# Performance work log

Measured on AMD Instinct MI355X. Metric: run time of the kernel, lower is better.

## Reference

```python
import jax, jax.numpy as jnp
import numpy as np
import math

EPS = 1e-6
NOISE = 1e-5

def _icnn(x, w0r, b0, w1r, b1, zw, g0r, g1r, ob):
    # x: [..., D]; returns [..., P, D]
    w0 = jax.nn.softplus(w0r) ** 2            # [P, 2D, D]
    w1 = jax.nn.softplus(w1r) ** 2            # [P, D, 2D]
    g0 = jax.nn.sigmoid(g0r)[:, None]          # [P, 1]
    g1 = jax.nn.sigmoid(g1r)[:, None]
    z0 = jax.nn.softplus((jnp.einsum('...d,pkd->...pk', x, w0) + b0) * g0)  # [..., P, 2D]
    xw1 = jnp.einsum('...pk,pdk->...pd', z0, w1) + b1                        # [..., P, D]
    zmap = jnp.einsum('...pk,pkd->...pd', z0, zw)
    z1 = jax.nn.softplus(xw1 * g1 + zmap)
    return z1 + ob

def _convex_gate(x, gw, gb):
    u = jax.nn.softplus(jnp.einsum('...d,od->...o', x, gw) + gb)
    return 1.0 - jnp.exp(-u)  # [..., 1]

def _scalar_hull(x, w0r, b0, w1r, b1, zw, g0r, g1r, ob, gw, gb, key):
    g = _convex_gate(x, gw, gb)
    xg = (x + jax.random.normal(key, x.shape, x.dtype) * NOISE) * g
    r = jnp.sqrt(jnp.mean(xg * xg, axis=-1, keepdims=True) + EPS)
    tau = jnp.exp(0.30343 * r + 0.22159)
    scores = _icnn(xg, w0r, b0, w1r, b1, zw, g0r, g1r, ob).mean(-1)  # [..., P]
    lse = jax.nn.logsumexp(scores * tau, axis=-1, keepdims=True)
    return jnp.squeeze(lse / tau, -1)

def _mixer(q, k, v, mask, qp, kp, whq, whk):
    keys = jax.random.split(jax.random.key(42), 6)
    gate_q = jax.nn.softplus(q)
    q = q * gate_q
    r = jnp.sqrt(jnp.mean(q * q, axis=-1, keepdims=True) + EPS)  # [B,H,S,1]
    tau = jnp.exp(0.30343 * r + 0.22159)
    fq = _scalar_hull(q, *qp, keys[0])  # [B,H,S]
    gk = _scalar_hull(k, *kp, keys[1])
    # creative: perturbed dual evaluations, detached delta
    qn = (jax.random.uniform(keys[2], q.shape, q.dtype) - 0.5) * NOISE
    kn = (jax.random.uniform(keys[3], k.shape, k.dtype) - 0.5) * NOISE
    fq_ = _scalar_hull(q + qn, *qp, keys[4])
    gk_ = _scalar_hull(k + kn, *kp, keys[5])
    fq = fq - 0.1 * jax.lax.stop_gradient(fq_ - fq)
    gk = gk - 0.1 * jax.lax.stop_gradient(gk_ - gk)
    phi_q = jax.nn.softplus(jnp.minimum(jnp.einsum('bhsd,rd->bhsr', q, whq), 20.0))
    phi_k = jax.nn.softplus(jnp.minimum(jnp.einsum('bhsd,rd->bhsr', k, whk), 20.0))
    # LSE_r(log(phi_q+eps) + log(phi_k+eps)) == log((phi_q+eps) @ (phi_k+eps)^T), exactly
    logK = jnp.log(jnp.einsum('bhir,bhjr->bhij', phi_q + EPS, phi_k + EPS))
    scores = fq[..., None] + gk[..., None, :] + logK + jnp.log(jnp.maximum(mask, EPS))
    logits = scores * tau  # tau [B,H,S,1] broadcasts over keys
    log_w = logits - jax.nn.logsumexp(logits, axis=-1, keepdims=True)
    w = jnp.exp(log_w)
    out = jnp.einsum('bhij,bhjd->bhid', w, v)
    a = jax.nn.softmax(w.sum(-3), axis=-1).mean(1)  # [B, S]
    mn = a.min(-1, keepdims=True)
    mx = a.max(-1, keepdims=True)
    a = (a - mn) / (mx - mn + EPS)
    return out, a

def setup_inputs() -> dict:
    B, H, S, D, P, R = 2, 8, 1024, 64, 8, 16
    d1 = 2 * D
    key = jax.random.key(0)
    ks = jax.random.split(key, 32)
    mean0 = math.log(math.sqrt(2.0 / D))
    mean1 = math.log(math.sqrt(2.0 / d1))
    def hull_params(i):
        kk = jax.random.split(ks[i], 6)
        return dict(
            w0=mean0 + 0.2 * jax.random.normal(kk[0], (P, d1, D)),
            b0=jnp.zeros((P, d1)),
            w1=mean1 + 0.2 * jax.random.normal(kk[1], (P, D, d1)),
            b1=jnp.zeros((P, D)),
            zw=jax.random.uniform(kk[2], (P, d1, D), minval=-1.0, maxval=1.0) / math.sqrt(d1 * D) * math.sqrt(6.0),
            g0=jnp.full((P,), -3.0),
            g1=jnp.full((P,), -3.0),
            ob=jnp.zeros((P, D)),
            gw=jax.random.normal(kk[3], (1, D)) / math.sqrt(D),
            gb=jnp.zeros((1,)),
        )
    qp = hull_params(10)
    kp = hull_params(11)
    inp = {
        'q': jax.random.normal(ks[0], (B, H, S, D)),
        'k': jax.random.normal(ks[1], (B, H, S, D)),
        'v': jax.random.normal(ks[2], (B, H, S, D)),
        'mask': jax.random.uniform(ks[3], (B, H, S, S)),
        'whq': jax.random.normal(ks[4], (R, D)) / math.sqrt(D),
        'whk': jax.random.normal(ks[5], (R, D)) / math.sqrt(D),
    }
    for name, p in (('q', qp), ('k', kp)):
        for pn, pv in p.items():
            inp[f'{name}_{pn}'] = pv
    return inp

def reference(q, k, v, mask,
              q_w0, q_b0, q_w1, q_b1, q_zw, q_g0, q_g1, q_ob, q_gw, q_gb,
              k_w0, k_b0, k_w1, k_b1, k_zw, k_g0, k_g1, k_ob, k_gw, k_gb,
              whq, whk):
    qp = (q_w0, q_b0, q_w1, q_b1, q_zw, q_g0, q_g1, q_ob, q_gw, q_gb)
    kp = (k_w0, k_b0, k_w1, k_b1, k_zw, k_g0, k_g1, k_ob, k_gw, k_gb)
    return _mixer(q, k, v, mask, qp, kp, whq, whk)
```

## Files before the change

kernel.cpp:

```cpp
#include <hip/hip_runtime.h>
#include <hip/hip_bf16.h>
#include <math.h>

typedef __hip_bfloat16 bf16;
typedef __attribute__((ext_vector_type(8))) short short8;
typedef __attribute__((ext_vector_type(4))) float f32x4;
#define EPSF 1e-6f

__device__ __forceinline__ float b2f(bf16 v){ return __bfloat162float(v); }
__device__ __forceinline__ bf16  f2b(float v){ return __float2bfloat16(v); }
__device__ __forceinline__ float spf(float x){ return x > 20.f ? x : __logf(1.f + __expf(x)); }
__device__ __forceinline__ float sigf(float x){ return 1.f/(1.f + __expf(-x)); }

__device__ __forceinline__ float wsum(float v){
#pragma unroll
  for (int m = 32; m; m >>= 1) v += __shfl_xor(v, m, 64);
  return v;
}
__device__ __forceinline__ float wmaxr(float v){
#pragma unroll
  for (int m = 32; m; m >>= 1) v = fmaxf(v, __shfl_xor(v, m, 64));
  return v;
}
__device__ __forceinline__ float wminr(float v){
#pragma unroll
  for (int m = 32; m; m >>= 1) v = fminf(v, __shfl_xor(v, m, 64));
  return v;
}

struct PrepArgs {
  const float* w0r[2]; const float* b0[2]; const float* w1r[2]; const float* b1[2];
  const float* zw[2];  const float* g0[2]; const float* g1[2]; const float* ob[2];
  bf16* W0gB[2]; bf16* MtB[2]; float* b0g[2]; float* B1g[2]; float* obm[2];
};

__global__ __launch_bounds__(256) void prep_kernel(PrepArgs a){
  int idx = blockIdx.x*256 + threadIdx.x;
  int s = idx >> 16, r = idx & 65535;
  {
    int p = r >> 13;
    float g0 = sigf(a.g0[s][p]);
    float w  = spf(a.w0r[s][r]);
    a.W0gB[s][r] = f2b(g0 * w * w);
  }
  {
    int pd = r >> 7, kk = r & 127;
    int p = pd >> 6, d = pd & 63;
    float g1 = sigf(a.g1[s][p]);
    float w  = spf(a.w1r[s][r]);
    float z  = a.zw[s][(p<<13) + (kk<<6) + d];
    a.MtB[s][r] = f2b(g1 * w * w + z);
  }
  if (r < 1024) a.b0g[s][r] = sigf(a.g0[s][r>>7]) * a.b0[s][r];
  if (r < 512)  a.B1g[s][r] = sigf(a.g1[s][r>>6]) * a.b1[s][r];
  if (r < 8) {
    float t = 0.f;
    for (int d = 0; d < 64; ++d) t += a.ob[s][r*64 + d];
    a.obm[s][r] = t * (1.f/64.f);
  }
}

struct HullArgs {
  const float* x[2]; const float* gw[2]; const float* gb[2]; const float* wh[2];
  const bf16* W0gB[2]; const bf16* MtB[2];
  const float* b0g[2]; const float* B1g[2]; const float* obm[2];
  float* tauOut; float* fOut[2]; float* phiOut[2];
};

__global__ __launch_bounds__(256) void hull_kernel(HullArgs A){
  __shared__ __align__(16) bf16 xgb[16][72];
  __shared__ __align__(16) bf16 z0[16][1032];
  __shared__ float tauh[16];
  __shared__ float scoreb[16][8];
  int bid = blockIdx.x;
  int s = bid >> 10;
  int isQ = (s == 0);
  long row0 = (long)(bid & 1023) * 16;
  const float* x   = A.x[s];
  const float* gw  = A.gw[s];
  const float* wh  = A.wh[s];
  const bf16* W0gB = A.W0gB[s];
  const bf16* MtB  = A.MtB[s];
  const float* b0g = A.b0g[s];
  const float* B1g = A.B1g[s];
  const float* obm = A.obm[s];
  float* fOut   = A.fOut[s];
  float* phiOut = A.phiOut[s];
  int t = threadIdx.x, lane = t & 63, w = t >> 6;
  float gbf = A.gb[s][0];

  for (int rp = 0; rp < 4; ++rp) {
    int r = rp*4 + w;
    long row = row0 + r;
    float xv = x[row*64 + lane];
    float xh = isQ ? xv * spf(xv) : xv;
    float s1 = wsum(xh * gw[lane]);
    float g = 1.f - __expf(-spf(s1 + gbf));
    float xgv = xh * g;
    float msq = wsum(xgv*xgv)*(1.f/64.f) + EPSF;
    float th = __expf(0.30343f*sqrtf(msq) + 0.22159f);
    if (lane == 0) tauh[r] = th;
    if (isQ) {
      float m2 = wsum(xh*xh)*(1.f/64.f) + EPSF;
      if (lane == 0) A.tauOut[row] = __expf(0.30343f*sqrtf(m2) + 0.22159f);
    }
    xgb[r][lane] = f2b(xgv);
    float myphi = 0.f;
#pragma unroll
    for (int jj = 0; jj < 16; ++jj) {
      float pv = wsum(xh * wh[jj*64 + lane]);
      if (lane == jj) myphi = pv;
    }
    if (lane < 16) phiOut[row*16 + lane] = spf(fminf(myphi, 20.f)) + EPSF;
  }
  __syncthreads();

  {
    int g = lane >> 4, cl = lane & 15;
    short8 a0 = *(const short8*)&xgb[cl][g*8];
    short8 a1 = *(const short8*)&xgb[cl][32 + g*8];
    for (int ct = 0; ct < 16; ++ct) {
      int col = w*256 + ct*16 + cl;
      const short8* bp = (const short8*)(W0gB + col*64);
      short8 b0 = bp[g];
      short8 b1 = bp[4 + g];
      f32x4 acc = {0.f, 0.f, 0.f, 0.f};
      acc = __builtin_amdgcn_mfma_f32_16x16x32_bf16(a0, b0, acc, 0, 0, 0);
      acc = __builtin_amdgcn_mfma_f32_16x16x32_bf16(a1, b1, acc, 0, 0, 0);
      float bb = b0g[col];
#pragma unroll
      for (int rg = 0; rg < 4; ++rg)
        z0[g*4 + rg][col] = f2b(spf(acc[rg] + bb));
    }
  }
  __syncthreads();

  {
    int g = lane >> 4, cl = lane & 15;
    for (int pi = 0; pi < 2; ++pi) {
      int p = w + pi*4;
      short8 af[4];
#pragma unroll
      for (int kc = 0; kc < 4; ++kc)
        af[kc] = *(const short8*)&z0[cl][p*128 + kc*32 + g*8];
      float s0 = 0.f, s1 = 0.f, s2 = 0.f, s3 = 0.f;
#pragma unroll
      for (int nt = 0; nt < 4; ++nt) {
        int dcol = nt*16 + cl;
        const short8* mp = (const short8*)(MtB + (p*64 + dcol)*128);
        f32x4 acc = {0.f, 0.f, 0.f, 0.f};
#pragma unroll
        for (int kc = 0; kc < 4; ++kc)
          acc = __builtin_amdgcn_mfma_f32_16x16x32_bf16(af[kc], mp[kc*4 + g], acc, 0, 0, 0);
        float bb = B1g[p*64 + dcol];
        s0 += spf(acc[0] + bb);
        s1 += spf(acc[1] + bb);
        s2 += spf(acc[2] + bb);
        s3 += spf(acc[3] + bb);
      }
#pragma unroll
      for (int m = 1; m < 16; m <<= 1) {
        s0 += __shfl_xor(s0, m, 64);
        s1 += __shfl_xor(s1, m, 64);
        s2 += __shfl_xor(s2, m, 64);
        s3 += __shfl_xor(s3, m, 64);
      }
      if (cl == 0) {
        scoreb[g*4+0][p] = s0 * (1.f/64.f);
        scoreb[g*4+1][p] = s1 * (1.f/64.f);
        scoreb[g*4+2][p] = s2 * (1.f/64.f);
        scoreb[g*4+3][p] = s3 * (1.f/64.f);
      }
    }
  }
  __syncthreads();

  if (t < 16) {
    int r = t;
    float th = tauh[r];
    float li[8]; float m = -1e30f;
#pragma unroll
    for (int p = 0; p < 8; ++p) { li[p] = (scoreb[r][p] + obm[p]) * th; m = fmaxf(m, li[p]); }
    float ssum = 0.f;
#pragma unroll
    for (int p = 0; p < 8; ++p) ssum += __expf(li[p] - m);
    fOut[row0 + r] = (m + __logf(ssum)) / th;
  }
}

__global__ __launch_bounds__(512) void attn2_kernel(
  const float* __restrict__ mask, const float* __restrict__ vv,
  const float* __restrict__ phiQ, const float* __restrict__ phiK,
  const float* __restrict__ fqA, const float* __restrict__ gkA, const float* __restrict__ tauA,
  float* __restrict__ eBuf, float* __restrict__ outO)
{
  __shared__ __align__(16) float lg[8][1024];
  __shared__ __align__(16) float pvp[8][2][64];
  __shared__ float phq[16][16];
  __shared__ float fqs[16], taus[16], sinvL[8];
  int t = threadIdx.x, lane = t & 63, w = t >> 6;
  int b = blockIdx.x >> 9, it = blockIdx.x & 511;
  int i0 = it * 2;

  if (t < 256) { int row = t>>4, jj = t&15;
    phq[row][jj] = phiQ[((long)(b*8 + (row>>1))*1024 + i0 + (row&1))*16 + jj]; }
  else if (t < 272) { int row = t-256;
    fqs[row] = fqA[(long)(b*8 + (row>>1))*1024 + i0 + (row&1)]; }
  else if (t < 288) { int row = t-272;
    taus[row] = tauA[(long)(b*8 + (row>>1))*1024 + i0 + (row&1)]; }
  __syncthreads();

  int hl = w & 3, rr = w >> 2;
  int lrow = hl*2 + rr;
  int wr = t >> 8;
  int wj4 = (t & 255) * 4;
  float* wrow = eBuf + ((long)b*1024 + i0 + wr)*1024 + wj4;

  for (int g = 0; g < 2; ++g) {
    int h = g*4 + hl;
    int bh = b*8 + h;
    int grow = g*8 + lrow;

    if (g > 0) {
      int r = t >> 6, d = t & 63;
      int hh = (g-1)*4 + (r >> 1), rrow = r & 1;
      outO[((long)(b*8 + hh)*1024 + i0 + rrow)*64 + d] =
        pvp[r][0][d] + pvp[r][1][d];
    }

    {
      float pq[16];
#pragma unroll
      for (int c = 0; c < 16; ++c) pq[c] = phq[grow][c];
      float fq = fqs[grow], ta = taus[grow];
      const float* pkb = phiK + (long)bh*16384;
      const float* mrow = mask + ((long)bh*1024 + i0 + rr)*1024;
      const float* gkb = gkA + (long)bh*1024;
#pragma unroll 2
      for (int jj = 0; jj < 16; ++jj) {
        int j = jj*64 + lane;
        const float4* pk = (const float4*)(pkb + j*16);
        float4 k0 = pk[0], k1 = pk[1], k2 = pk[2], k3 = pk[3];
        float dp = pq[0]*k0.x + pq[1]*k0.y + pq[2]*k0.z + pq[3]*k0.w
                 + pq[4]*k1.x + pq[5]*k1.y + pq[6]*k1.z + pq[7]*k1.w
                 + pq[8]*k2.x + pq[9]*k2.y + pq[10]*k2.z + pq[11]*k2.w
                 + pq[12]*k3.x + pq[13]*k3.y + pq[14]*k3.z + pq[15]*k3.w;
        float mk = fmaxf(mrow[j], EPSF);
        float sc = fq + gkb[j] + __logf(dp * mk);
        lg[lrow][j] = sc * ta;
      }
    }
    {
      float m = -1e30f;
#pragma unroll
      for (int c = 0; c < 16; ++c) m = fmaxf(m, lg[lrow][c*64 + lane]);
      m = wmaxr(m);
      float s = 0.f;
#pragma unroll
      for (int c = 0; c < 16; ++c) {
        float e = __expf(lg[lrow][c*64 + lane] - m);
        lg[lrow][c*64 + lane] = e;
        s += e;
      }
      s = wsum(s);
      if (lane == 0) sinvL[lrow] = 1.f / s;
    }
    __syncthreads();

    {
      float4 acc;
      if (g == 0) acc = make_float4(0.f,0.f,0.f,0.f);
      else        acc = *(const float4*)wrow;
#pragma unroll
      for (int q = 0; q < 4; ++q) {
        float sv = sinvL[q*2 + wr];
        float4 e = *(const float4*)&lg[q*2 + wr][wj4];
        acc.x += sv*e.x; acc.y += sv*e.y; acc.z += sv*e.z; acc.w += sv*e.w;
      }
      *(float4*)wrow = acc;
    }
    {
      int d4 = lane & 15, jg = lane >> 4;
      int r0 = hl*2, r1 = r0 + 1;
      float si0 = sinvL[r0], si1 = sinvL[r1];
      const float* vb = vv + (long)bh*65536 + d4*4;
      float4 a0 = make_float4(0.f,0.f,0.f,0.f);
      float4 a1 = make_float4(0.f,0.f,0.f,0.f);
      int jbase = rr*512 + jg;
#pragma unroll 4
      for (int jt = 0; jt < 128; ++jt) {
        int j = jbase + jt*4;
        float4 vf = *(const float4*)(vb + (long)j*64);
        float p0 = lg[r0][j], p1 = lg[r1][j];
        a0.x += p0*vf.x; a0.y += p0*vf.y; a0.z += p0*vf.z; a0.w += p0*vf.w;
        a1.x += p1*vf.x; a1.y += p1*vf.y; a1.z += p1*vf.z; a1.w += p1*vf.w;
      }
      a0.x += __shfl_xor(a0.x,16,64); a0.y += __shfl_xor(a0.y,16,64);
      a0.z += __shfl_xor(a0.z,16,64); a0.w += __shfl_xor(a0.w,16,64);
      a0.x += __shfl_xor(a0.x,32,64); a0.y += __shfl_xor(a0.y,32,64);
      a0.z += __shfl_xor(a0.z,32,64); a0.w += __shfl_xor(a0.w,32,64);
      a1.x += __shfl_xor(a1.x,16,64); a1.y += __shfl_xor(a1.y,16,64);
      a1.z += __shfl_xor(a1.z,16,64); a1.w += __shfl_xor(a1.w,16,64);
      a1.x += __shfl_xor(a1.x,32,64); a1.y += __shfl_xor(a1.y,32,64);
      a1.z += __shfl_xor(a1.z,32,64); a1.w += __shfl_xor(a1.w,32,64);
      if (jg == 0) {
        float4 o0 = make_float4(a0.x*si0, a0.y*si0, a0.z*si0, a0.w*si0);
        float4 o1 = make_float4(a1.x*si1, a1.y*si1, a1.z*si1, a1.w*si1);
        *(float4*)&pvp[r0][rr][d4*4] = o0;
        *(float4*)&pvp[r1][rr][d4*4] = o1;
      }
    }
    __syncthreads();
  }

  {
    int r = t >> 6, d = t & 63;
    int hh = 4 + (r >> 1), rrow = r & 1;
    outO[((long)(b*8 + hh)*1024 + i0 + rrow)*64 + d] =
      pvp[r][0][d] + pvp[r][1][d];
  }
}

__global__ __launch_bounds__(256) void asoft_kernel(const float* __restrict__ wsAtt, float* __restrict__ aAcc){
  int b = blockIdx.x >> 5, ii = blockIdx.x & 31;
  int t = threadIdx.x, lane = t & 63, w = t >> 6;
  __shared__ float redm[4], reds[4];
  float a0 = 0.f, a1 = 0.f, a2 = 0.f, a3 = 0.f;
  for (int i = 0; i < 32; ++i) {
    const float* wr = wsAtt + ((long)b*1024 + ii*32 + i)*1024;
    float4 v = *(const float4*)(wr + t*4);
    float m = fmaxf(fmaxf(v.x, v.y), fmaxf(v.z, v.w));
    m = wmaxr(m);
    if (lane == 0) redm[w] = m;
    __syncthreads();
    m = fmaxf(fmaxf(redm[0], redm[1]), fmaxf(redm[2], redm[3]));
    float4 e;
    e.x = __expf(v.x - m); e.y = __expf(v.y - m); e.z = __expf(v.z - m); e.w = __expf(v.w - m);
    float s = e.x + e.y + e.z + e.w;
    s = wsum(s);
    if (lane == 0) reds[w] = s;
    __syncthreads();
    s = reds[0] + reds[1] + reds[2] + reds[3];
    float inv = 1.f / (s * 1024.f);
    a0 += e.x*inv; a1 += e.y*inv; a2 += e.z*inv; a3 += e.w*inv;
    __syncthreads();
  }
  atomicAdd(&aAcc[b*1024 + t*4+0], a0);
  atomicAdd(&aAcc[b*1024 + t*4+1], a1);
  atomicAdd(&aAcc[b*1024 + t*4+2], a2);
  atomicAdd(&aAcc[b*1024 + t*4+3], a3);
}

__global__ __launch_bounds__(1024) void anorm_kernel(const float* __restrict__ aAcc, float* __restrict__ outA){
  int b = blockIdx.x, t = threadIdx.x, lane = t & 63, w = t >> 6;
  float v = aAcc[b*1024 + t];
  __shared__ float rmn[16], rmx[16];
  float mn = wminr(v), mx = wmaxr(v);
  if (lane == 0) { rmn[w] = mn; rmx[w] = mx; }
  __syncthreads();
  mn = rmn[0]; mx = rmx[0];
#pragma unroll
  for (int i = 1; i < 16; ++i) { mn = fminf(mn, rmn[i]); mx = fmaxf(mx, rmx[i]); }
  outA[b*1024 + t] = (v - mn) / (mx - mn + EPSF);
}

extern "C" void kernel_launch(void* const* d_in, const int* in_sizes, int n_in,
                              void* d_out, int out_size, void* d_ws, size_t ws_size,
                              hipStream_t stream)
{
  (void)in_sizes; (void)n_in; (void)out_size; (void)ws_size;
  const float* q    = (const float*)d_in[0];
  const float* k    = (const float*)d_in[1];
  const float* v    = (const float*)d_in[2];
  const float* mask = (const float*)d_in[3];
  const float* whq  = (const float*)d_in[4];
  const float* whk  = (const float*)d_in[5];

  float* ws = (float*)d_ws;
  bf16* w0b_q = (bf16*)(ws);
  bf16* w0b_k = (bf16*)(ws + 32768);
  bf16* mtb_q = (bf16*)(ws + 65536);
  bf16* mtb_k = (bf16*)(ws + 98304);
  float* b0g_q = ws + 131072;
  float* b0g_k = ws + 132096;
  float* B1g_q = ws + 133120;
  float* B1g_k = ws + 133632;
  float* obm_q = ws + 134144;
  float* obm_k = ws + 134160;
  float* tau_q = ws + 134176;
  float* fq_a  = ws + 150560;
  float* gk_a  = ws + 166944;
  float* phi_q = ws + 183328;
  float* phi_k = ws + 445472;
  float* e_buf = ws + 707616;
  float* a_acc = ws + 2804768;

  hipMemsetAsync(a_acc, 0, 2048*sizeof(float), stream);

  PrepArgs pa;
  for (int s = 0; s < 2; ++s) {
    int o = 6 + 10*s;
    pa.w0r[s] = (const float*)d_in[o+0];
    pa.b0 [s] = (const float*)d_in[o+1];
    pa.w1r[s] = (const float*)d_in[o+2];
    pa.b1 [s] = (const float*)d_in[o+3];
    pa.zw [s] = (const float*)d_in[o+4];
    pa.g0 [s] = (const float*)d_in[o+5];
    pa.g1 [s] = (const float*)d_in[o+6];
    pa.ob [s] = (const float*)d_in[o+7];
  }
  pa.W0gB[0]=w0b_q; pa.W0gB[1]=w0b_k; pa.MtB[0]=mtb_q; pa.MtB[1]=mtb_k;
  pa.b0g[0]=b0g_q; pa.b0g[1]=b0g_k; pa.B1g[0]=B1g_q; pa.B1g[1]=B1g_k;
  pa.obm[0]=obm_q; pa.obm[1]=obm_k;

  prep_kernel<<<512,256,0,stream>>>(pa);

  HullArgs ha;
  ha.x[0] = q; ha.x[1] = k;
  ha.gw[0] = (const float*)d_in[14]; ha.gw[1] = (const float*)d_in[24];
  ha.gb[0] = (const float*)d_in[15]; ha.gb[1] = (const float*)d_in[25];
  ha.wh[0] = whq; ha.wh[1] = whk;
  ha.W0gB[0] = w0b_q; ha.W0gB[1] = w0b_k;
  ha.MtB[0] = mtb_q;  ha.MtB[1] = mtb_k;
  ha.b0g[0] = b0g_q;  ha.b0g[1] = b0g_k;
  ha.B1g[0] = B1g_q;  ha.B1g[1] = B1g_k;
  ha.obm[0] = obm_q;  ha.obm[1] = obm_k;
  ha.tauOut = tau_q;
  ha.fOut[0] = fq_a;  ha.fOut[1] = gk_a;
  ha.phiOut[0] = phi_q; ha.phiOut[1] = phi_k;

  hull_kernel<<<2048,256,0,stream>>>(ha);

  attn2_kernel<<<1024,512,0,stream>>>(mask, v, phi_q, phi_k, fq_a, gk_a, tau_q,
                                      e_buf, (float*)d_out);
  asoft_kernel<<<64,256,0,stream>>>(e_buf, a_acc);
  anorm_kernel<<<2,1024,0,stream>>>(a_acc, (float*)d_out + 1048576);
}
```

Before: 264.1 us.

## Fuse head-mean softmax into attention kernel and use bf16 MFMA for PV

Restructures attention so each block handles 8 query rows across all 8 heads. The head-averaged attention map is accumulated in shared memory and its second softmax is done in place. This removes the global eBuf round trip and the separate asoft kernel. The P·V product now runs on MFMA 16x16x32 bf16 using a transposed bf16 copy of V made by a new prep kernel. Exponentials are stored as bf16, which lowers precision. The grid also shrinks from 1024 to 256 blocks, which may hurt occupancy, and the extra V transpose pass adds some memory traffic.

```diff
diff --git a/kernel.cpp b/kernel.cpp
--- a/kernel.cpp
+++ b/kernel.cpp
@@ -26,6 +26,11 @@
 #pragma unroll
   for (int m = 32; m; m >>= 1) v = fminf(v, __shfl_xor(v, m, 64));
   return v;
+}
+__device__ __forceinline__ void unp(float fv, float& lo, float& hi){
+  unsigned u = __float_as_uint(fv);
+  lo = __uint_as_float(u << 16);
+  hi = __uint_as_float(u & 0xffff0000u);
 }
 
 struct PrepArgs {
@@ -57,6 +62,23 @@
     float t = 0.f;
     for (int d = 0; d < 64; ++d) t += a.ob[s][r*64 + d];
     a.obm[s][r] = t * (1.f/64.f);
+  }
+}
+
+__global__ __launch_bounds__(256) void vprep_kernel(const float* __restrict__ v, bf16* __restrict__ vT){
+  __shared__ float vL[64][65];
+  int bh = blockIdx.x >> 4, jt = blockIdx.x & 15;
+  int j0 = jt * 64, t = threadIdx.x;
+  for (int i = 0; i < 16; ++i) {
+    int idx = t + i*256;
+    int jj = idx >> 6, d = idx & 63;
+    vL[jj][d] = v[((long)bh*1024 + j0 + jj)*64 + d];
+  }
+  __syncthreads();
+  for (int i = 0; i < 16; ++i) {
+    int idx = t + i*256;
+    int dd = idx >> 6, js = idx & 63;
+    vT[((long)bh*64 + dd)*1024 + j0 + js] = f2b(vL[js][dd]);
   }
 }
 
@@ -188,57 +210,46 @@
   }
 }
 
-__global__ __launch_bounds__(512) void attn2_kernel(
-  const float* __restrict__ mask, const float* __restrict__ vv,
+__global__ __launch_bounds__(512) void attn3_kernel(
+  const float* __restrict__ mask, const bf16* __restrict__ vT,
   const float* __restrict__ phiQ, const float* __restrict__ phiK,
   const float* __restrict__ fqA, const float* __restrict__ gkA, const float* __restrict__ tauA,
-  float* __restrict__ eBuf, float* __restrict__ outO)
+  float* __restrict__ aAcc, float* __restrict__ outO)
 {
-  __shared__ __align__(16) float lg[8][1024];
-  __shared__ __align__(16) float pvp[8][2][64];
-  __shared__ float phq[16][16];
-  __shared__ float fqs[16], taus[16], sinvL[8];
+  __shared__ __align__(16) bf16 ebf[16][1032];
+  __shared__ __align__(16) float sm[8][1024];
+  __shared__ float phq[8][16];
+  __shared__ float fqs[8], taus[8], sinvL[8];
   int t = threadIdx.x, lane = t & 63, w = t >> 6;
-  int b = blockIdx.x >> 9, it = blockIdx.x & 511;
-  int i0 = it * 2;
-
-  if (t < 256) { int row = t>>4, jj = t&15;
-    phq[row][jj] = phiQ[((long)(b*8 + (row>>1))*1024 + i0 + (row&1))*16 + jj]; }
-  else if (t < 272) { int row = t-256;
-    fqs[row] = fqA[(long)(b*8 + (row>>1))*1024 + i0 + (row&1)]; }
-  else if (t < 288) { int row = t-272;
-    taus[row] = tauA[(long)(b*8 + (row>>1))*1024 + i0 + (row&1)]; }
-  __syncthreads();
-
-  int hl = w & 3, rr = w >> 2;
-  int lrow = hl*2 + rr;
-  int wr = t >> 8;
-  int wj4 = (t & 255) * 4;
-  float* wrow = eBuf + ((long)b*1024 + i0 + wr)*1024 + wj4;
-
-  for (int g = 0; g < 2; ++g) {
-    int h = g*4 + hl;
+  int b = blockIdx.x >> 7, it = blockIdx.x & 127;
+  int i0 = it * 8;
+
+  {
+    float* z = (float*)&ebf[8][0];
+    for (int idx = t; idx < 4128; idx += 512) z[idx] = 0.f;
+  }
+
+  for (int h = 0; h < 8; ++h) {
     int bh = b*8 + h;
-    int grow = g*8 + lrow;
-
-    if (g > 0) {
-      int r = t >> 6, d = t & 63;
-      int hh = (g-1)*4 + (r >> 1), rrow = r & 1;
-      outO[((long)(b*8 + hh)*1024 + i0 + rrow)*64 + d] =
-        pvp[r][0][d] + pvp[r][1][d];
-    }
-
+    long pbase = (long)bh * 1024;
+    if (t < 128) { int r = t >> 4, c = t & 15;
+      phq[r][c] = phiQ[(pbase + i0 + r)*16 + c]; }
+    else if (t < 136) { int r = t - 128; fqs[r] = fqA[pbase + i0 + r]; }
+    else if (t < 144) { int r = t - 136; taus[r] = tauA[pbase + i0 + r]; }
+    __syncthreads();
+
+    float l[16];
     {
       float pq[16];
 #pragma unroll
-      for (int c = 0; c < 16; ++c) pq[c] = phq[grow][c];
-      float fq = fqs[grow], ta = taus[grow];
-      const float* pkb = phiK + (long)bh*16384;
-      const float* mrow = mask + ((long)bh*1024 + i0 + rr)*1024;
-      const float* gkb = gkA + (long)bh*1024;
+      for (int c = 0; c < 16; ++c) pq[c] = phq[w][c];
+      float fq = fqs[w], ta = taus[w];
+      const float* pkb = phiK + pbase*16;
+      const float* mrow = mask + (pbase + i0 + w)*1024;
+      const float* gkb = gkA + pbase;
 #pragma unroll 2
-      for (int jj = 0; jj < 16; ++jj) {
-        int j = jj*64 + lane;
+      for (int c = 0; c < 16; ++c) {
+        int j = c*64 + lane;
         const float4* pk = (const float4*)(pkb + j*16);
         float4 k0 = pk[0], k1 = pk[1], k2 = pk[2], k3 = pk[3];
         float dp = pq[0]*k0.x + pq[1]*k0.y + pq[2]*k0.z + pq[3]*k0.w
@@ -246,109 +257,88 @@
                  + pq[8]*k2.x + pq[9]*k2.y + pq[10]*k2.z + pq[11]*k2.w
                  + pq[12]*k3.x + pq[13]*k3.y + pq[14]*k3.z + pq[15]*k3.w;
         float mk = fmaxf(mrow[j], EPSF);
-        float sc = fq + gkb[j] + __logf(dp * mk);
-        lg[lrow][j] = sc * ta;
+        l[c] = (fq + gkb[j] + __logf(dp * mk)) * ta;
       }
     }
     {
       float m = -1e30f;
 #pragma unroll
-      for (int c = 0; c < 16; ++c) m = fmaxf(m, lg[lrow][c*64 + lane]);
+      for (int c = 0; c < 16; ++c) m = fmaxf(m, l[c]);
       m = wmaxr(m);
       float s = 0.f;
 #pragma unroll
       for (int c = 0; c < 16; ++c) {
-        float e = __expf(lg[lrow][c*64 + lane] - m);
-        lg[lrow][c*64 + lane] = e;
+        float e = __expf(l[c] - m);
         s += e;
+        ebf[w][c*64 + lane] = f2b(e);
       }
       s = wsum(s);
-      if (lane == 0) sinvL[lrow] = 1.f / s;
+      if (lane == 0) sinvL[w] = 1.f / s;
     }
     __syncthreads();
 
-    {
-      float4 acc;
-      if (g == 0) acc = make_float4(0.f,0.f,0.f,0.f);
-      else        acc = *(const float4*)wrow;
-#pragma unroll
-      for (int q = 0; q < 4; ++q) {
-        float sv = sinvL[q*2 + wr];
-        float4 e = *(const float4*)&lg[q*2 + wr][wj4];
-        acc.x += sv*e.x; acc.y += sv*e.y; acc.z += sv*e.z; acc.w += sv*e.w;
-      }
-      *(float4*)wrow = acc;
-    }
-    {
-      int d4 = lane & 15, jg = lane >> 4;
-      int r0 = hl*2, r1 = r0 + 1;
-      float si0 = sinvL[r0], si1 = sinvL[r1];
-      const float* vb = vv + (long)bh*65536 + d4*4;
-      float4 a0 = make_float4(0.f,0.f,0.f,0.f);
-      float4 a1 = make_float4(0.f,0.f,0.f,0.f);
-      int jbase = rr*512 + jg;
-#pragma unroll 4
-      for (int jt = 0; jt < 128; ++jt) {
-        int j = jbase + jt*4;
-        float4 vf = *(const float4*)(vb + (long)j*64);
-        float p0 = lg[r0][j], p1 = lg[r1][j];
-        a0.x += p0*vf.x; a0.y += p0*vf.y; a0.z += p0*vf.z; a0.w += p0*vf.w;
-        a1.x += p1*vf.x; a1.y += p1*vf.y; a1.z += p1*vf.z; a1.w += p1*vf.w;
-      }
-      a0.x += __shfl_xor(a0.x,16,64); a0.y += __shfl_xor(a0.y,16,64);
-      a0.z += __shfl_xor(a0.z,16,64); a0.w += __shfl_xor(a0.w,16,64);
-      a0.x += __shfl_xor(a0.x,32,64); a0.y += __shfl_xor(a0.y,32,64);
-      a0.z += __shfl_xor(a0.z,32,64); a0.w += __shfl_xor(a0.w,32,64);
-      a1.x += __shfl_xor(a1.x,16,64); a1.y += __shfl_xor(a1.y,16,64);
-      a1.z += __shfl_xor(a1.z,16,64); a1.w += __shfl_xor(a1.w,16,64);
-      a1.x += __shfl_xor(a1.x,32,64); a1.y += __shfl_xor(a1.y,32,64);
-      a1.z += __shfl_xor(a1.z,32,64); a1.w += __shfl_xor(a1.w,32,64);
-      if (jg == 0) {
-        float4 o0 = make_float4(a0.x*si0, a0.y*si0, a0.z*si0, a0.w*si0);
-        float4 o1 = make_float4(a1.x*si1, a1.y*si1, a1.z*si1, a1.w*si1);
-        *(float4*)&pvp[r0][rr][d4*4] = o0;
-        *(float4*)&pvp[r1][rr][d4*4] = o1;
+    if (w < 4) {
+      int g = lane >> 4, cl = lane & 15;
+      const short8* bp = (const short8*)(vT + ((long)bh*64 + w*16 + cl)*1024);
+      f32x4 cf = {0.f, 0.f, 0.f, 0.f};
+      for (int kc = 0; kc < 32; ++kc) {
+        short8 aF = *(const short8*)&ebf[cl][kc*32 + g*8];
+        short8 bF = bp[kc*4 + g];
+        cf = __builtin_amdgcn_mfma_f32_16x16x32_bf16(aF, bF, cf, 0, 0, 0);
+      }
+      if (g < 2) {
+#pragma unroll
+        for (int i = 0; i < 4; ++i) {
+          int row = g*4 + i;
+          outO[(pbase + i0 + row)*64 + w*16 + cl] = cf[i] * sinvL[row];
+        }
+      }
+    } else {
+      int r0 = (w-4)*2;
+#pragma unroll
+      for (int rr = 0; rr < 2; ++rr) {
+        int r = r0 + rr;
+        float sv = sinvL[r];
+#pragma unroll
+        for (int ch = 0; ch < 4; ++ch) {
+          int jb = ch*256 + lane*4;
+          uint2 eb = *(const uint2*)&ebf[r][jb];
+          float e0,e1,e2,e3;
+          unp(__uint_as_float(eb.x), e0, e1);
+          unp(__uint_as_float(eb.y), e2, e3);
+          float4 acc;
+          if (h == 0) acc = make_float4(0.f,0.f,0.f,0.f);
+          else        acc = *(float4*)&sm[r][jb];
+          acc.x += sv*e0; acc.y += sv*e1; acc.z += sv*e2; acc.w += sv*e3;
+          *(float4*)&sm[r][jb] = acc;
+        }
       }
     }
     __syncthreads();
   }
 
   {
-    int r = t >> 6, d = t & 63;
-    int hh = 4 + (r >> 1), rrow = r & 1;
-    outO[((long)(b*8 + hh)*1024 + i0 + rrow)*64 + d] =
-      pvp[r][0][d] + pvp[r][1][d];
-  }
-}
-
-__global__ __launch_bounds__(256) void asoft_kernel(const float* __restrict__ wsAtt, float* __restrict__ aAcc){
-  int b = blockIdx.x >> 5, ii = blockIdx.x & 31;
-  int t = threadIdx.x, lane = t & 63, w = t >> 6;
-  __shared__ float redm[4], reds[4];
-  float a0 = 0.f, a1 = 0.f, a2 = 0.f, a3 = 0.f;
-  for (int i = 0; i < 32; ++i) {
-    const float* wr = wsAtt + ((long)b*1024 + ii*32 + i)*1024;
-    float4 v = *(const float4*)(wr + t*4);
-    float m = fmaxf(fmaxf(v.x, v.y), fmaxf(v.z, v.w));
+    float l2[16];
+    float m = -1e30f;
+#pragma unroll
+    for (int c = 0; c < 16; ++c) { l2[c] = sm[w][c*64 + lane]; m = fmaxf(m, l2[c]); }
     m = wmaxr(m);
-    if (lane == 0) redm[w] = m;
-    __syncthreads();
-    m = fmaxf(fmaxf(redm[0], redm[1]), fmaxf(redm[2], redm[3]));
-    float4 e;
-    e.x = __expf(v.x - m); e.y = __expf(v.y - m); e.z = __expf(v.z - m); e.w = __expf(v.w - m);
-    float s = e.x + e.y + e.z + e.w;
+    float s = 0.f;
+#pragma unroll
+    for (int c = 0; c < 16; ++c) { l2[c] = __expf(l2[c] - m); s += l2[c]; }
     s = wsum(s);
-    if (lane == 0) reds[w] = s;
-    __syncthreads();
-    s = reds[0] + reds[1] + reds[2] + reds[3];
-    float inv = 1.f / (s * 1024.f);
-    a0 += e.x*inv; a1 += e.y*inv; a2 += e.z*inv; a3 += e.w*inv;
-    __syncthreads();
-  }
-  atomicAdd(&aAcc[b*1024 + t*4+0], a0);
-  atomicAdd(&aAcc[b*1024 + t*4+1], a1);
-  atomicAdd(&aAcc[b*1024 + t*4+2], a2);
-  atomicAdd(&aAcc[b*1024 + t*4+3], a3);
+    float sc = 1.f / (s * 1024.f);
+#pragma unroll
+    for (int c = 0; c < 16; ++c)
+      sm[w][c*64 + lane] = l2[c] * sc;
+  }
+  __syncthreads();
+  for (int j = t; j < 1024; j += 512) {
+    float ssum = 0.f;
+#pragma unroll
+    for (int r = 0; r < 8; ++r) ssum += sm[r][j];
+    atomicAdd(&aAcc[b*1024 + j], ssum);
+  }
 }
 
 __global__ __launch_bounds__(1024) void anorm_kernel(const float* __restrict__ aAcc, float* __restrict__ outA){
@@ -392,8 +382,8 @@
   float* gk_a  = ws + 166944;
   float* phi_q = ws + 183328;
   float* phi_k = ws + 445472;
-  float* e_buf = ws + 707616;
-  float* a_acc = ws + 2804768;
+  bf16*  v_T   = (bf16*)(ws + 707616);
+  float* a_acc = ws + 1231904;
 
   hipMemsetAsync(a_acc, 0, 2048*sizeof(float), stream);
 
@@ -414,6 +404,7 @@
   pa.obm[0]=obm_q; pa.obm[1]=obm_k;
 
   prep_kernel<<<512,256,0,stream>>>(pa);
+  vprep_kernel<<<256,256,0,stream>>>(v, v_T);
 
   HullArgs ha;
   ha.x[0] = q; ha.x[1] = k;
@@ -431,8 +422,7 @@
 
   hull_kernel<<<2048,256,0,stream>>>(ha);
 
-  attn2_kernel<<<1024,512,0,stream>>>(mask, v, phi_q, phi_k, fq_a, gk_a, tau_q,
-                                      e_buf, (float*)d_out);
-  asoft_kernel<<<64,256,0,stream>>>(e_buf, a_acc);
+  attn3_kernel<<<256,512,0,stream>>>(mask, v_T, phi_q, phi_k, fq_a, gk_a, tau_q,
+                                     a_acc, (float*)d_out);
   anorm_kernel<<<2,1024,0,stream>>>(a_acc, (float*)d_out + 1048576);
 }
```

New measurement: 228.4 us. 13.5% less time.
